# Kernel optimization log

Hardware: AMD Instinct MI355X
Metric: run time of the kernel (lower is better)

## Reference

```python
import jax, jax.numpy as jnp
import numpy as np

N = 100000
E = 1600000
BN_EPS = 1e-5
# (in_channels, heads, out_channels, concat) per GATv2 layer
LAYERS = [(22, 3, 18, True), (54, 3, 14, True), (42, 3, 12, True), (36, 5, 10, False)]


def setup_inputs() -> dict:
    key = jax.random.key(0)
    ks = iter(jax.random.split(key, 64))
    nrm = lambda shape, s=0.1: jax.random.normal(next(ks), shape, jnp.float32) * s
    d = {}
    d["x"] = jax.random.normal(next(ks), (N, 22), jnp.float32)
    d["edge_index"] = jax.random.randint(next(ks), (2, E), 0, N)
    for i, (cin, h, c, concat) in enumerate(LAYERS, 1):
        d[f"Wl{i}"] = nrm((cin, h * c))
        d[f"Wr{i}"] = nrm((cin, h * c))
        d[f"bl{i}"] = jnp.zeros((h * c,), jnp.float32)
        d[f"br{i}"] = jnp.zeros((h * c,), jnp.float32)
        d[f"att{i}"] = nrm((h, c))
        outd = h * c if concat else c
        d[f"b{i}"] = jnp.zeros((outd,), jnp.float32)
        d[f"g{i}"] = jnp.ones((outd,), jnp.float32)
        d[f"be{i}"] = jnp.zeros((outd,), jnp.float32)
        d[f"rm{i}"] = nrm((outd,))
        d[f"rv{i}"] = jax.random.uniform(next(ks), (outd,), jnp.float32, 0.5, 1.5)
    d["Wmu"] = nrm((10, 10)); d["bmu"] = jnp.zeros((10,), jnp.float32)
    d["Wlv"] = nrm((10, 10)); d["blv"] = jnp.zeros((10,), jnp.float32)
    return d


def _gatv2(x, Wl, Wr, bl, br, att, b, src, dst, H, C, concat):
    n = x.shape[0]
    xl = (x @ Wl + bl).reshape(n, H, C)  # source transform (also the message)
    xr = (x @ Wr + br).reshape(n, H, C)  # target transform
    m = jax.nn.leaky_relu(xl[src] + xr[dst], 0.2)          # [Etot, H, C]
    e = jnp.einsum('ehc,hc->eh', m, att)                   # [Etot, H]
    emax = jax.lax.stop_gradient(jax.ops.segment_max(e, dst, num_segments=n))
    ex = jnp.exp(e - emax[dst])
    den = jax.ops.segment_sum(ex, dst, num_segments=n)     # [n, H]
    alpha = ex / den[dst]
    out = jax.ops.segment_sum(xl[src] * alpha[..., None], dst, num_segments=n)
    out = out.reshape(n, H * C) if concat else out.mean(axis=1)
    return out + b


def _bn(x, g, be, rm, rv):
    return g * (x - rm) * jax.lax.rsqrt(rv + BN_EPS) + be


def _fwd(p, edge_index):
    n = p["x"].shape[0]
    loop = jnp.arange(n)  # PyG GATv2Conv adds self-loops by default
    src = jnp.concatenate([edge_index[0], loop])
    dst = jnp.concatenate([edge_index[1], loop])
    h = p["x"]
    for i, (cin, H, C, concat) in enumerate(LAYERS, 1):
        h = _gatv2(h, p[f"Wl{i}"], p[f"Wr{i}"], p[f"bl{i}"], p[f"br{i}"],
                   p[f"att{i}"], p[f"b{i}"], src, dst, H, C, concat)
        h = _bn(h, p[f"g{i}"], p[f"be{i}"], p[f"rm{i}"], p[f"rv{i}"])
        if i == 1:  # source applies ELU only after bn1
            h = jax.nn.elu(h)
    mu = h @ p["Wmu"] + p["bmu"]
    log_var = h @ p["Wlv"] + p["blv"]
    return mu, log_var


def reference(x, edge_index, Wl1, Wr1, bl1, br1, att1, b1, g1, be1, rm1, rv1, Wl2, Wr2, bl2, br2, att2, b2, g2, be2, rm2, rv2, Wl3, Wr3, bl3, br3, att3, b3, g3, be3, rm3, rv3, Wl4, Wr4, bl4, br4, att4, b4, g4, be4, rm4, rv4, Wmu, bmu, Wlv, blv):
    p = {k: v for k, v in locals().items() if k != "edge_index"}
    return _fwd(p, edge_index)
```

## Files before the change

kernel.cpp:

```cpp
#include <hip/hip_runtime.h>

#define BN_EPS 1e-5f

typedef _Float16 half_t;
typedef _Float16 half2_t __attribute__((ext_vector_type(2)));

#define NBK_MAX 512
#define EPB 8192
#define REC 64
#define CAP 5120

#if __has_builtin(__builtin_amdgcn_fdot2)
#define DOT2(a, b, c) __builtin_amdgcn_fdot2((a), (b), (c), false)
#else
#define DOT2(a, b, c) fmaf((float)(a).x, (float)(b).x, fmaf((float)(a).y, (float)(b).y, (c)))
#endif


__global__ void __launch_bounds__(256) bucket_scatter_kernel(
    const int* __restrict__ ei, int* __restrict__ bcur, unsigned* __restrict__ bstage,
    int E, int etot, int nbk) {
  __shared__ int lh[NBK_MAX], lbase[NBK_MAX];
  int base = blockIdx.x * EPB;
  int cnt = min(EPB, etot - base);
  for (int i = threadIdx.x; i < nbk; i += 256) lh[i] = 0;
  __syncthreads();
  for (int i = threadIdx.x; i < cnt; i += 256) {
    int e = base + i;
    int d = (e < E) ? ei[E + e] : (e - E);
    atomicAdd(&lh[d >> 8], 1);
  }
  __syncthreads();
  for (int i = threadIdx.x; i < nbk; i += 256) {
    int c = lh[i];
    lbase[i] = c ? (i * CAP + atomicAdd(&bcur[i], c)) : 0;
    lh[i] = 0;
  }
  __syncthreads();
  for (int i = threadIdx.x; i < cnt; i += 256) {
    int e = base + i;
    int s, d;
    if (e < E) { s = ei[e]; d = ei[E + e]; } else { s = e - E; d = s; }
    int b = d >> 8;
    int r = atomicAdd(&lh[b], 1);
    bstage[lbase[b] + r] = ((unsigned)s << 8) | (unsigned)(d & 255);
  }
}

__global__ void __launch_bounds__(256) csr_finalize_kernel(
    const unsigned* __restrict__ bstage, const int* __restrict__ bcur,
    int* __restrict__ start, int* __restrict__ deg, int* __restrict__ csrc, int n) {
  __shared__ int ld[256];
  __shared__ int wsum[4];
  int b = blockIdx.x, tid = threadIdx.x;
  int d0 = b << 8;
  int p0 = b * CAP;
  int bc = bcur[b];
  ld[tid] = 0;
  __syncthreads();
  for (int p = p0 + tid; p < p0 + bc; p += 256)
    atomicAdd(&ld[bstage[p] & 255u], 1);
  __syncthreads();
  int v = ld[tid];
  int lane = tid & 63, wid = tid >> 6;
  int incl = v;
#pragma unroll
  for (int off = 1; off < 64; off <<= 1) {
    int t = __shfl_up(incl, off, 64);
    if (lane >= off) incl += t;
  }
  if (lane == 63) wsum[wid] = incl;
  __syncthreads();
  if (tid == 0) {
    int s = 0;
#pragma unroll
    for (int w = 0; w < 4; w++) { int t = wsum[w]; wsum[w] = s; s += t; }
  }
  __syncthreads();
  incl += wsum[wid];
  int st = p0 + incl - v;
  int i = d0 + tid;
  if (i < n) { start[i] = st; deg[i] = v; }
  __syncthreads();
  ld[tid] = st;
  __syncthreads();
  for (int p = p0 + tid; p < p0 + bc; p += 256) {
    unsigned sd = bstage[p];
    int pos = atomicAdd(&ld[sd & 255u], 1);
    csrc[pos] = (int)(sd >> 8);
  }
}


template <int CIN, int H, int C, int JT, typename IT>
__global__ void __launch_bounds__(256) transform_kernel(
    const IT* __restrict__ x, const float* __restrict__ Wl, const float* __restrict__ Wr,
    const float* __restrict__ bl, const float* __restrict__ br, half_t* __restrict__ xl,
    half_t* __restrict__ xr, int n) {
  constexpr int HC = H * C;
  constexpr int TPN = HC / JT;
  __shared__ float sW[2 * CIN * HC];
  for (int i = threadIdx.x; i < CIN * HC; i += blockDim.x) {
    sW[i] = Wl[i];
    sW[CIN * HC + i] = Wr[i];
  }
  __syncthreads();
  int idx = blockIdx.x * blockDim.x + threadIdx.x;
  if (idx >= n * TPN) return;
  int node = idx / TPN;
  int j0 = (idx - node * TPN) * JT;

  float al[JT], ar[JT];
#pragma unroll
  for (int jj = 0; jj < JT; jj++) {
    al[jj] = bl[j0 + jj];
    ar[jj] = br[j0 + jj];
  }
  float xrow[CIN];
  if constexpr (sizeof(IT) == 4) {
    const float2* xp = reinterpret_cast<const float2*>((const float*)x + (size_t)node * CIN);
#pragma unroll
    for (int k2 = 0; k2 < CIN / 2; k2++) {
      float2 v = xp[k2];
      xrow[2 * k2] = v.x;
      xrow[2 * k2 + 1] = v.y;
    }
  } else {
    const half2_t* xp = reinterpret_cast<const half2_t*>((const half_t*)x + (size_t)node * CIN);
#pragma unroll
    for (int k2 = 0; k2 < CIN / 2; k2++) {
      half2_t v = xp[k2];
      xrow[2 * k2] = (float)v.x;
      xrow[2 * k2 + 1] = (float)v.y;
    }
  }
#pragma unroll
  for (int k = 0; k < CIN; k++) {
    float xs = xrow[k];
#pragma unroll
    for (int jj = 0; jj < JT; jj++) {
      al[jj] = fmaf(xs, sW[k * HC + j0 + jj], al[jj]);
      ar[jj] = fmaf(xs, sW[CIN * HC + k * HC + j0 + jj], ar[jj]);
    }
  }
#pragma unroll
  for (int jj = 0; jj < JT; jj++) {
    int j = j0 + jj;
    xl[(size_t)node * REC + j] = (half_t)al[jj];
    xr[(size_t)node * HC + j] = (half_t)ar[jj];
  }
}


#define IDX(K) csrc[p0 + (((K) < cnt) ? (K) : cnt - 1)]

#define ROW(B, IR)                                                                  \
  {                                                                                 \
    const uint* xp_ = reinterpret_cast<const uint*>(xlh + (size_t)(IR) * REC);      \
    _Pragma("unroll") for (int i_ = 0; i_ < C2; i_++) B[i_] = xp_[i_];              \
  }

#define COMP_ROW(B, M)                                                              \
  {                                                                                 \
    const half2_t* hp_ = reinterpret_cast<const half2_t*>(B);                       \
    float e_ = 0.f;                                                                 \
    _Pragma("unroll") for (int i = 0; i < C2; i++) {                                \
      half2_t m_ = hp_[i] + xr_h[i];                                                \
      half2_t mp_ = __builtin_elementwise_max(m_, h2z);                             \
      half2_t mn_ = __builtin_elementwise_min(m_, h2z);                             \
      m_ = mp_ + mn_ * h2lk;                                                        \
      e_ = DOT2(att_h[i], m_, e_);                                                  \
    }                                                                               \
    float ex_ = ((M) < cnt) ? __expf(e_) : 0.f;                                     \
    den += ex_;                                                                     \
    half_t exs_ = (half_t)ex_;                                                      \
    half2_t exv_ = {exs_, exs_};                                                    \
    _Pragma("unroll") for (int i = 0; i < C2; i++) acc[i] += exv_ * hp_[i];         \
  }

template <int H, int C, int MODE>
__global__ void __launch_bounds__(256) edge_kernel(
    const half_t* __restrict__ xl, const half_t* __restrict__ xr,
    const int* __restrict__ start, const int* __restrict__ deg,
    const int* __restrict__ csrc, const float* __restrict__ att,
    const float* __restrict__ bias, const float* __restrict__ g,
    const float* __restrict__ be, const float* __restrict__ rm,
    const float* __restrict__ rv, half_t* __restrict__ out, int n) {
  constexpr int HC = H * C;
  constexpr int C2 = C / 2;
  int t = blockIdx.x * blockDim.x + threadIdx.x;
  if (t >= n * H) return;
  int node = t / H;
  int h = t - node * H;

  const half2_t h2z = {(half_t)0.f, (half_t)0.f};
  const half2_t h2lk = {(half_t)0.2f, (half_t)0.2f};

  half2_t xr_h[C2], att_h[C2], acc[C2];
  const half2_t* xrp = reinterpret_cast<const half2_t*>(xr + (size_t)node * HC + h * C);
#pragma unroll
  for (int i = 0; i < C2; i++) {
    xr_h[i] = xrp[i];
    att_h[i] = half2_t{(half_t)att[h * C + 2 * i], (half_t)att[h * C + 2 * i + 1]};
    acc[i] = h2z;
  }
  float den = 0.f;

  int p0 = start[node];
  int cnt = deg[node];
  const half_t* xlh = xl + h * C;

  uint B0[C2], B1[C2], B2[C2];
  int i0, i1, i2;
  i0 = IDX(0); i1 = IDX(1); i2 = IDX(2);
  ROW(B0, i0) ROW(B1, i1) ROW(B2, i2)
  i0 = IDX(3); i1 = IDX(4); i2 = IDX(5);
  int cnt3 = ((cnt + 2) / 3) * 3;
  for (int m = 0; m < cnt3; m += 3) {
    COMP_ROW(B0, m)     ROW(B0, i0) i0 = IDX(m + 6);
    COMP_ROW(B1, m + 1) ROW(B1, i1) i1 = IDX(m + 7);
    COMP_ROW(B2, m + 2) ROW(B2, i2) i2 = IDX(m + 8);
  }

  float inv = 1.f / den;
  uint* orow = reinterpret_cast<uint*>(out + (size_t)node * HC + h * C);
#pragma unroll
  for (int c2 = 0; c2 < C2; c2++) {
    half2_t ov;
#pragma unroll
    for (int q = 0; q < 2; q++) {
      float a = q ? (float)acc[c2].y : (float)acc[c2].x;
      float val = a * inv;
      if constexpr (MODE != 2) {
        int j = h * C + 2 * c2 + q;
        val += bias[j];
        float sc = g[j] * rsqrtf(rv[j] + BN_EPS);
        val = fmaf(sc, val - rm[j], be[j]);
        if constexpr (MODE == 1) val = (val > 0.f) ? val : expm1f(val);
      }
      if (q) ov.y = (half_t)val; else ov.x = (half_t)val;
    }
    orow[c2] = *reinterpret_cast<uint*>(&ov);
  }
}


__global__ void final_kernel(const half_t* __restrict__ r4, const float* __restrict__ b4,
                             const float* __restrict__ g4, const float* __restrict__ be4,
                             const float* __restrict__ rm4, const float* __restrict__ rv4,
                             const float* __restrict__ Wmu, const float* __restrict__ bmu,
                             const float* __restrict__ Wlv, const float* __restrict__ blv,
                             float* __restrict__ out, int n) {
  int node = blockIdx.x * blockDim.x + threadIdx.x;
  if (node >= n) return;
  float hsum[10];
#pragma unroll
  for (int c = 0; c < 10; c++) hsum[c] = 0.f;
  const half2_t* r = reinterpret_cast<const half2_t*>(r4 + (size_t)node * 50);
  float rv_[50];
#pragma unroll
  for (int i = 0; i < 25; i++) {
    half2_t v = r[i];
    rv_[2 * i] = (float)v.x;
    rv_[2 * i + 1] = (float)v.y;
  }
#pragma unroll
  for (int h = 0; h < 5; h++)
#pragma unroll
    for (int c = 0; c < 10; c++) hsum[c] += rv_[h * 10 + c];
  float hv[10];
#pragma unroll
  for (int c = 0; c < 10; c++) {
    float v = hsum[c] * 0.2f + b4[c];
    float sc = g4[c] * rsqrtf(rv4[c] + BN_EPS);
    hv[c] = fmaf(sc, v - rm4[c], be4[c]);
  }
#pragma unroll
  for (int j = 0; j < 10; j++) {
    float mu = bmu[j], lv = blv[j];
#pragma unroll
    for (int c = 0; c < 10; c++) {
      mu = fmaf(hv[c], Wmu[c * 10 + j], mu);
      lv = fmaf(hv[c], Wlv[c * 10 + j], lv);
    }
    out[(size_t)node * 10 + j] = mu;
    out[(size_t)n * 10 + (size_t)node * 10 + j] = lv;
  }
}


extern "C" void kernel_launch(void* const* d_in, const int* in_sizes, int n_in,
                              void* d_out, int out_size, void* d_ws, size_t ws_size,
                              hipStream_t stream) {
  const float* x = (const float*)d_in[0];
  const int* ei = (const int*)d_in[1];
  const int n = in_sizes[0] / 22;
  const int E = in_sizes[1] / 2;
  const int etot = E + n;
  const int nbk = (n + 255) >> 8;

  auto P = [&](int i) { return (const float*)d_in[i]; };

  char* ws = (char*)d_ws;
  size_t off = 0;
  auto alloc = [&](size_t bytes) -> void* {
    void* p = ws + off;
    off += (bytes + 255) & ~(size_t)255;
    return p;
  };
  half_t* xl = (half_t*)alloc((size_t)n * REC * 2);
  half_t* xr = (half_t*)alloc((size_t)n * 54 * 2);
  half_t* hb = (half_t*)alloc((size_t)n * 54 * 2);
  int* start = (int*)alloc((size_t)n * 4);
  int* deg = (int*)alloc((size_t)n * 4);
  int* csrc = (int*)alloc((size_t)nbk * CAP * 4);
  int* bcur = (int*)alloc((size_t)nbk * 4);
  unsigned* bstage = (unsigned*)xl;

  unsigned bb = (unsigned)((etot + EPB - 1) / EPB);
  unsigned nblk = (unsigned)((n + 255) / 256);

  hipMemsetAsync(bcur, 0, (size_t)nbk * 4, stream);
  bucket_scatter_kernel<<<bb, 256, 0, stream>>>(ei, bcur, bstage, E, etot, nbk);
  csr_finalize_kernel<<<(unsigned)nbk, 256, 0, stream>>>(bstage, bcur, start, deg, csrc, n);

  transform_kernel<22, 3, 18, 6, float><<<(unsigned)(((size_t)n * 9 + 255) / 256), 256, 0, stream>>>(
      x, P(2), P(3), P(4), P(5), xl, xr, n);
  edge_kernel<3, 18, 1><<<(unsigned)(((size_t)n * 3 + 255) / 256), 256, 0, stream>>>(
      xl, xr, start, deg, csrc, P(6), P(7), P(8), P(9), P(10), P(11), hb, n);

  transform_kernel<54, 3, 14, 6, half_t><<<(unsigned)(((size_t)n * 7 + 255) / 256), 256, 0, stream>>>(
      hb, P(12), P(13), P(14), P(15), xl, xr, n);
  edge_kernel<3, 14, 0><<<(unsigned)(((size_t)n * 3 + 255) / 256), 256, 0, stream>>>(
      xl, xr, start, deg, csrc, P(16), P(17), P(18), P(19), P(20), P(21), hb, n);

  transform_kernel<42, 3, 12, 6, half_t><<<(unsigned)(((size_t)n * 6 + 255) / 256), 256, 0, stream>>>(
      hb, P(22), P(23), P(24), P(25), xl, xr, n);
  edge_kernel<3, 12, 0><<<(unsigned)(((size_t)n * 3 + 255) / 256), 256, 0, stream>>>(
      xl, xr, start, deg, csrc, P(26), P(27), P(28), P(29), P(30), P(31), hb, n);

  transform_kernel<36, 5, 10, 10, half_t><<<(unsigned)(((size_t)n * 5 + 255) / 256), 256, 0, stream>>>(
      hb, P(32), P(33), P(34), P(35), xl, xr, n);
  edge_kernel<5, 10, 2><<<(unsigned)(((size_t)n * 5 + 255) / 256), 256, 0, stream>>>(
      xl, xr, start, deg, csrc, P(36), nullptr, nullptr, nullptr, nullptr, nullptr, hb, n);

  final_kernel<<<nblk, 256, 0, stream>>>(
      hb, P(37), P(38), P(39), P(40), P(41), P(42), P(43), P(44), P(45), (float*)d_out, n);
}
```

Baseline: 478.8 us.

## Split each node-head edge loop across 8 lanes with shuffle reduction

The edge aggregation kernel now gives each (node, head) pair a group of 8 threads instead of one. Each lane walks a strided subset of the neighbor list, prefetching the next index, and partial sums and denominators are combined with xor shuffles. The goal is more parallelism and memory-level concurrency for the gather across the ~17-edge average degree. In exchange, many lanes sit idle on low-degree nodes, the 3-deep software pipeline is dropped, and the half-precision partials add shuffle and reduction cost.

```diff
diff --git a/kernel.cpp b/kernel.cpp
--- a/kernel.cpp
+++ b/kernel.cpp
@@ -152,32 +152,6 @@
 }
 
 
-#define IDX(K) csrc[p0 + (((K) < cnt) ? (K) : cnt - 1)]
-
-#define ROW(B, IR)                                                                  \
-  {                                                                                 \
-    const uint* xp_ = reinterpret_cast<const uint*>(xlh + (size_t)(IR) * REC);      \
-    _Pragma("unroll") for (int i_ = 0; i_ < C2; i_++) B[i_] = xp_[i_];              \
-  }
-
-#define COMP_ROW(B, M)                                                              \
-  {                                                                                 \
-    const half2_t* hp_ = reinterpret_cast<const half2_t*>(B);                       \
-    float e_ = 0.f;                                                                 \
-    _Pragma("unroll") for (int i = 0; i < C2; i++) {                                \
-      half2_t m_ = hp_[i] + xr_h[i];                                                \
-      half2_t mp_ = __builtin_elementwise_max(m_, h2z);                             \
-      half2_t mn_ = __builtin_elementwise_min(m_, h2z);                             \
-      m_ = mp_ + mn_ * h2lk;                                                        \
-      e_ = DOT2(att_h[i], m_, e_);                                                  \
-    }                                                                               \
-    float ex_ = ((M) < cnt) ? __expf(e_) : 0.f;                                     \
-    den += ex_;                                                                     \
-    half_t exs_ = (half_t)ex_;                                                      \
-    half2_t exv_ = {exs_, exs_};                                                    \
-    _Pragma("unroll") for (int i = 0; i < C2; i++) acc[i] += exv_ * hp_[i];         \
-  }
-
 template <int H, int C, int MODE>
 __global__ void __launch_bounds__(256) edge_kernel(
     const half_t* __restrict__ xl, const half_t* __restrict__ xr,
@@ -188,10 +162,13 @@
     const float* __restrict__ rv, half_t* __restrict__ out, int n) {
   constexpr int HC = H * C;
   constexpr int C2 = C / 2;
+  constexpr int G = 8;
   int t = blockIdx.x * blockDim.x + threadIdx.x;
-  if (t >= n * H) return;
-  int node = t / H;
-  int h = t - node * H;
+  int gid = t >> 3;
+  if (gid >= n * H) return;
+  int gl = t & (G - 1);
+  int node = gid / H;
+  int h = gid - node * H;
 
   const half2_t h2z = {(half_t)0.f, (half_t)0.f};
   const half2_t h2lk = {(half_t)0.2f, (half_t)0.2f};
@@ -210,17 +187,48 @@
   int cnt = deg[node];
   const half_t* xlh = xl + h * C;
 
-  uint B0[C2], B1[C2], B2[C2];
-  int i0, i1, i2;
-  i0 = IDX(0); i1 = IDX(1); i2 = IDX(2);
-  ROW(B0, i0) ROW(B1, i1) ROW(B2, i2)
-  i0 = IDX(3); i1 = IDX(4); i2 = IDX(5);
-  int cnt3 = ((cnt + 2) / 3) * 3;
-  for (int m = 0; m < cnt3; m += 3) {
-    COMP_ROW(B0, m)     ROW(B0, i0) i0 = IDX(m + 6);
-    COMP_ROW(B1, m + 1) ROW(B1, i1) i1 = IDX(m + 7);
-    COMP_ROW(B2, m + 2) ROW(B2, i2) i2 = IDX(m + 8);
-  }
+  int trips = (cnt + G - 1) >> 3;
+  int m = gl;
+  int idx = csrc[p0 + min(m, cnt - 1)];
+  for (int tr = 0; tr < trips; tr++) {
+    uint B[C2];
+    const uint* xp = reinterpret_cast<const uint*>(xlh + (size_t)idx * REC);
+#pragma unroll
+    for (int i = 0; i < C2; i++) B[i] = xp[i];
+    int mn = m + G;
+    int idx_n = csrc[p0 + min(mn, cnt - 1)];
+
+    const half2_t* hp = reinterpret_cast<const half2_t*>(B);
+    float e = 0.f;
+#pragma unroll
+    for (int i = 0; i < C2; i++) {
+      half2_t mv = hp[i] + xr_h[i];
+      half2_t mp = __builtin_elementwise_max(mv, h2z);
+      half2_t mnn = __builtin_elementwise_min(mv, h2z);
+      mv = mp + mnn * h2lk;
+      e = DOT2(att_h[i], mv, e);
+    }
+    float ex = (m < cnt) ? __expf(e) : 0.f;
+    den += ex;
+    half_t exs = (half_t)ex;
+    half2_t exv = {exs, exs};
+#pragma unroll
+    for (int i = 0; i < C2; i++) acc[i] += exv * hp[i];
+
+    m = mn;
+    idx = idx_n;
+  }
+
+#pragma unroll
+  for (int mask = 1; mask < G; mask <<= 1) {
+    den += __shfl_xor(den, mask, 64);
+#pragma unroll
+    for (int i = 0; i < C2; i++) {
+      int sv = __shfl_xor(__builtin_bit_cast(int, acc[i]), mask, 64);
+      acc[i] += __builtin_bit_cast(half2_t, sv);
+    }
+  }
+  if (gl != 0) return;
 
   float inv = 1.f / den;
   uint* orow = reinterpret_cast<uint*>(out + (size_t)node * HC + h * C);
@@ -326,22 +334,22 @@
 
   transform_kernel<22, 3, 18, 6, float><<<(unsigned)(((size_t)n * 9 + 255) / 256), 256, 0, stream>>>(
       x, P(2), P(3), P(4), P(5), xl, xr, n);
-  edge_kernel<3, 18, 1><<<(unsigned)(((size_t)n * 3 + 255) / 256), 256, 0, stream>>>(
+  edge_kernel<3, 18, 1><<<(unsigned)(((size_t)n * 24 + 255) / 256), 256, 0, stream>>>(
       xl, xr, start, deg, csrc, P(6), P(7), P(8), P(9), P(10), P(11), hb, n);
 
   transform_kernel<54, 3, 14, 6, half_t><<<(unsigned)(((size_t)n * 7 + 255) / 256), 256, 0, stream>>>(
       hb, P(12), P(13), P(14), P(15), xl, xr, n);
-  edge_kernel<3, 14, 0><<<(unsigned)(((size_t)n * 3 + 255) / 256), 256, 0, stream>>>(
+  edge_kernel<3, 14, 0><<<(unsigned)(((size_t)n * 24 + 255) / 256), 256, 0, stream>>>(
       xl, xr, start, deg, csrc, P(16), P(17), P(18), P(19), P(20), P(21), hb, n);
 
   transform_kernel<42, 3, 12, 6, half_t><<<(unsigned)(((size_t)n * 6 + 255) / 256), 256, 0, stream>>>(
       hb, P(22), P(23), P(24), P(25), xl, xr, n);
-  edge_kernel<3, 12, 0><<<(unsigned)(((size_t)n * 3 + 255) / 256), 256, 0, stream>>>(
+  edge_kernel<3, 12, 0><<<(unsigned)(((size_t)n * 24 + 255) / 256), 256, 0, stream>>>(
       xl, xr, start, deg, csrc, P(26), P(27), P(28), P(29), P(30), P(31), hb, n);
 
   transform_kernel<36, 5, 10, 10, half_t><<<(unsigned)(((size_t)n * 5 + 255) / 256), 256, 0, stream>>>(
       hb, P(32), P(33), P(34), P(35), xl, xr, n);
-  edge_kernel<5, 10, 2><<<(unsigned)(((size_t)n * 5 + 255) / 256), 256, 0, stream>>>(
+  edge_kernel<5, 10, 2><<<(unsigned)(((size_t)n * 40 + 255) / 256), 256, 0, stream>>>(
       xl, xr, start, deg, csrc, P(36), nullptr, nullptr, nullptr, nullptr, nullptr, hb, n);
 
   final_kernel<<<nblk, 256, 0, stream>>>(
```

Result: slower. 534.5 us (+11.7%).

## Split each node-head edge aggregation across two lanes with shuffle reduction

Applied to the files above, without the earlier changes.

Each (node, head) pair in the GATv2 edge kernel is now handled by two adjacent threads. Each thread takes alternating neighbours from the CSR list, and the partial softmax denominators and fp16 accumulators are then combined with an xor shuffle. This doubles the thread count and halves the per-thread serial gather chain, aiming for more memory-level parallelism across 17 neighbours per node on average. The cost is extra shuffles, idle second lanes during the epilogue, and more wavefronts competing for registers.

```diff
diff --git a/kernel.cpp b/kernel.cpp
--- a/kernel.cpp
+++ b/kernel.cpp
@@ -152,7 +152,7 @@
 }
 
 
-#define IDX(K) csrc[p0 + (((K) < cnt) ? (K) : cnt - 1)]
+#define PIDX(K) csrc[p0 + gl + 2 * (((K) < cnt_l) ? (K) : cnt_l - 1)]
 
 #define ROW(B, IR)                                                                  \
   {                                                                                 \
@@ -171,7 +171,7 @@
       m_ = mp_ + mn_ * h2lk;                                                        \
       e_ = DOT2(att_h[i], m_, e_);                                                  \
     }                                                                               \
-    float ex_ = ((M) < cnt) ? __expf(e_) : 0.f;                                     \
+    float ex_ = ((M) < cnt_l) ? __expf(e_) : 0.f;                                   \
     den += ex_;                                                                     \
     half_t exs_ = (half_t)ex_;                                                      \
     half2_t exv_ = {exs_, exs_};                                                    \
@@ -189,9 +189,11 @@
   constexpr int HC = H * C;
   constexpr int C2 = C / 2;
   int t = blockIdx.x * blockDim.x + threadIdx.x;
-  if (t >= n * H) return;
-  int node = t / H;
-  int h = t - node * H;
+  int gid = t >> 1;
+  if (gid >= n * H) return;
+  int gl = t & 1;
+  int node = gid / H;
+  int h = gid - node * H;
 
   const half2_t h2z = {(half_t)0.f, (half_t)0.f};
   const half2_t h2lk = {(half_t)0.2f, (half_t)0.2f};
@@ -208,19 +210,30 @@
 
   int p0 = start[node];
   int cnt = deg[node];
+  int cnt_l = (cnt > gl) ? ((cnt - gl + 1) >> 1) : 0;
   const half_t* xlh = xl + h * C;
 
-  uint B0[C2], B1[C2], B2[C2];
-  int i0, i1, i2;
-  i0 = IDX(0); i1 = IDX(1); i2 = IDX(2);
-  ROW(B0, i0) ROW(B1, i1) ROW(B2, i2)
-  i0 = IDX(3); i1 = IDX(4); i2 = IDX(5);
-  int cnt3 = ((cnt + 2) / 3) * 3;
-  for (int m = 0; m < cnt3; m += 3) {
-    COMP_ROW(B0, m)     ROW(B0, i0) i0 = IDX(m + 6);
-    COMP_ROW(B1, m + 1) ROW(B1, i1) i1 = IDX(m + 7);
-    COMP_ROW(B2, m + 2) ROW(B2, i2) i2 = IDX(m + 8);
-  }
+  if (cnt_l > 0) {
+    uint B0[C2], B1[C2], B2[C2];
+    int i0, i1, i2;
+    i0 = PIDX(0); i1 = PIDX(1); i2 = PIDX(2);
+    ROW(B0, i0) ROW(B1, i1) ROW(B2, i2)
+    i0 = PIDX(3); i1 = PIDX(4); i2 = PIDX(5);
+    int cnt3 = ((cnt_l + 2) / 3) * 3;
+    for (int m = 0; m < cnt3; m += 3) {
+      COMP_ROW(B0, m)     ROW(B0, i0) i0 = PIDX(m + 6);
+      COMP_ROW(B1, m + 1) ROW(B1, i1) i1 = PIDX(m + 7);
+      COMP_ROW(B2, m + 2) ROW(B2, i2) i2 = PIDX(m + 8);
+    }
+  }
+
+  den += __shfl_xor(den, 1, 64);
+#pragma unroll
+  for (int i = 0; i < C2; i++) {
+    int sv = __shfl_xor(__builtin_bit_cast(int, acc[i]), 1, 64);
+    acc[i] += __builtin_bit_cast(half2_t, sv);
+  }
+  if (gl != 0) return;
 
   float inv = 1.f / den;
   uint* orow = reinterpret_cast<uint*>(out + (size_t)node * HC + h * C);
@@ -326,22 +339,22 @@
 
   transform_kernel<22, 3, 18, 6, float><<<(unsigned)(((size_t)n * 9 + 255) / 256), 256, 0, stream>>>(
       x, P(2), P(3), P(4), P(5), xl, xr, n);
-  edge_kernel<3, 18, 1><<<(unsigned)(((size_t)n * 3 + 255) / 256), 256, 0, stream>>>(
+  edge_kernel<3, 18, 1><<<(unsigned)(((size_t)n * 6 + 255) / 256), 256, 0, stream>>>(
       xl, xr, start, deg, csrc, P(6), P(7), P(8), P(9), P(10), P(11), hb, n);
 
   transform_kernel<54, 3, 14, 6, half_t><<<(unsigned)(((size_t)n * 7 + 255) / 256), 256, 0, stream>>>(
       hb, P(12), P(13), P(14), P(15), xl, xr, n);
-  edge_kernel<3, 14, 0><<<(unsigned)(((size_t)n * 3 + 255) / 256), 256, 0, stream>>>(
+  edge_kernel<3, 14, 0><<<(unsigned)(((size_t)n * 6 + 255) / 256), 256, 0, stream>>>(
       xl, xr, start, deg, csrc, P(16), P(17), P(18), P(19), P(20), P(21), hb, n);
 
   transform_kernel<42, 3, 12, 6, half_t><<<(unsigned)(((size_t)n * 6 + 255) / 256), 256, 0, stream>>>(
       hb, P(22), P(23), P(24), P(25), xl, xr, n);
-  edge_kernel<3, 12, 0><<<(unsigned)(((size_t)n * 3 + 255) / 256), 256, 0, stream>>>(
+  edge_kernel<3, 12, 0><<<(unsigned)(((size_t)n * 6 + 255) / 256), 256, 0, stream>>>(
       xl, xr, start, deg, csrc, P(26), P(27), P(28), P(29), P(30), P(31), hb, n);
 
   transform_kernel<36, 5, 10, 10, half_t><<<(unsigned)(((size_t)n * 5 + 255) / 256), 256, 0, stream>>>(
       hb, P(32), P(33), P(34), P(35), xl, xr, n);
-  edge_kernel<5, 10, 2><<<(unsigned)(((size_t)n * 5 + 255) / 256), 256, 0, stream>>>(
+  edge_kernel<5, 10, 2><<<(unsigned)(((size_t)n * 10 + 255) / 256), 256, 0, stream>>>(
       xl, xr, start, deg, csrc, P(36), nullptr, nullptr, nullptr, nullptr, nullptr, hb, n);
 
   final_kernel<<<nblk, 256, 0, stream>>>(
```

New measurement: 488.1 us. No clear change (+2.0%).
